# Kernel tuning notes

Hardware: AMD Instinct MI355X
Metric: run time of the kernel (lower is better)

## Reference

```python
import jax, jax.numpy as jnp
import numpy as np

NUM_REGIONS = 32  # region ids 1..32; id 0 is background, excluded like torch.unique()[ids>0]


def setup_inputs() -> dict:
    key = jax.random.key(0)
    k1, k2 = jax.random.split(key)
    B, T, C, D, H, W = 2, 8, 64, 48, 48, 48
    features = jax.random.normal(k1, (B, T, C, D, H, W), dtype=jnp.float32)
    segmentation = jax.random.randint(k2, (B, 1, D, H, W), 0, NUM_REGIONS + 1, dtype=jnp.int32)
    return {"features": features, "segmentation": segmentation}


def reference(features, segmentation):
    # features: [B, T, C, D, H, W], segmentation: [B, 1, D, H, W] (int region ids)
    B, T, C, D, H, W = features.shape
    N = D * H * W
    seg = segmentation.reshape(B, N)                 # [B, N]
    feats = features.reshape(B, T, C, N)             # [B, T, C, N]

    def per_batch(f, s):
        # f: [T, C, N], s: [N]
        fv = f.reshape(T * C, N).T                   # [N, T*C] voxel-major
        sums = jax.ops.segment_sum(fv, s, num_segments=NUM_REGIONS + 1)          # [R+1, T*C]
        counts = jax.ops.segment_sum(jnp.ones((N,), f.dtype), s,
                                     num_segments=NUM_REGIONS + 1)               # [R+1]
        # mean per region; empty regions stay zero (torch code `continue`s, leaving zeros)
        means = jnp.where(counts[:, None] > 0,
                          sums / jnp.maximum(counts, 1.0)[:, None],
                          0.0)
        return means[1:].reshape(NUM_REGIONS, T, C).transpose(1, 0, 2)           # [T, R, C]

    return jax.vmap(per_batch)(feats, seg)          # [B, T, num_regions, feature_dim]
```

## Files before the change

### kernel.cpp

```cpp
#include <hip/hip_runtime.h>


#define BB 2
#define TT 8
#define CC 64
#define NVOX 110592
#define NREG 32
#define RS 33
#define TS 67
#define WTILE (16*TS)
#define WACC (RS*CC)
#define WLDS (WTILE+WACC)
#define VPW 256
#define CHUNKV 1024

__global__ __launch_bounds__(256) void seg_hist(const int* __restrict__ seg,
                                                float* __restrict__ counts) {
    __shared__ float h[4 * RS];
    const int tid = threadIdx.x;
    const int w = tid >> 6;
    for (int i = tid; i < 4 * RS; i += 256) h[i] = 0.f;
    __syncthreads();

    const int base = blockIdx.x * 1024 + tid * 4;
    const int b = base / NVOX;
    const int4 s4 = *(const int4*)(seg + base);
    atomicAdd(&h[w * RS + s4.x], 1.f);
    atomicAdd(&h[w * RS + s4.y], 1.f);
    atomicAdd(&h[w * RS + s4.z], 1.f);
    atomicAdd(&h[w * RS + s4.w], 1.f);
    __syncthreads();

    if (tid < RS) {
        const float v = h[tid] + h[RS + tid] + h[2 * RS + tid] + h[3 * RS + tid];
        atomicAdd(&counts[b * RS + tid], v);
    }
}

__global__ __launch_bounds__(256) void seg_sum(const float* __restrict__ feat,
                                               const int* __restrict__ seg,
                                               float* __restrict__ out) {
    __shared__ float s[4 * WLDS];
    const int tid = threadIdx.x;
    const int w = tid >> 6;
    const int l = tid & 63;
    const int b = blockIdx.z;
    const int t = blockIdx.y;

    float* __restrict__ tile = s + w * WLDS;
    float* __restrict__ acc = tile + WTILE;
    #pragma unroll
    for (int i = l; i < WACC; i += 64) acc[i] = 0.f;

    const int v0 = blockIdx.x * CHUNKV + w * VPW;
    const int cq = l >> 2;
    const int iq = l & 3;
    const float* __restrict__ fbt = feat + (size_t)(b * TT + t) * CC * NVOX + v0;
    const float* __restrict__ fp0 = fbt + (size_t)(cq) * NVOX + iq * 4;
    const float* __restrict__ fp1 = fbt + (size_t)(cq + 16) * NVOX + iq * 4;
    const float* __restrict__ fp2 = fbt + (size_t)(cq + 32) * NVOX + iq * 4;
    const float* __restrict__ fp3 = fbt + (size_t)(cq + 48) * NVOX + iq * 4;
    const int* __restrict__ sb = seg + (size_t)b * NVOX + v0;

    const int wb = (iq * 4) * TS + cq;

    #pragma unroll 2
    for (int tj = 0; tj < 16; ++tj) {
        const int vo = tj * 16;
        const float4 f0 = *(const float4*)(fp0 + vo);
        const float4 f1 = *(const float4*)(fp1 + vo);
        const float4 f2 = *(const float4*)(fp2 + vo);
        const float4 f3 = *(const float4*)(fp3 + vo);
        const int4 s0 = *(const int4*)(sb + vo);
        const int4 s1 = *(const int4*)(sb + vo + 4);
        const int4 s2 = *(const int4*)(sb + vo + 8);
        const int4 s3 = *(const int4*)(sb + vo + 12);

        __builtin_amdgcn_wave_barrier();
        tile[wb] = f0.x;           tile[wb + TS] = f0.y;
        tile[wb + 2 * TS] = f0.z;  tile[wb + 3 * TS] = f0.w;
        tile[wb + 16] = f1.x;          tile[wb + 16 + TS] = f1.y;
        tile[wb + 16 + 2 * TS] = f1.z; tile[wb + 16 + 3 * TS] = f1.w;
        tile[wb + 32] = f2.x;          tile[wb + 32 + TS] = f2.y;
        tile[wb + 32 + 2 * TS] = f2.z; tile[wb + 32 + 3 * TS] = f2.w;
        tile[wb + 48] = f3.x;          tile[wb + 48 + TS] = f3.y;
        tile[wb + 48 + 2 * TS] = f3.z; tile[wb + 48 + 3 * TS] = f3.w;
        __builtin_amdgcn_wave_barrier();

        const int rv[16] = {s0.x, s0.y, s0.z, s0.w, s1.x, s1.y, s1.z, s1.w,
                            s2.x, s2.y, s2.z, s2.w, s3.x, s3.y, s3.z, s3.w};
        #pragma unroll
        for (int v = 0; v < 16; ++v) {
            const float val = tile[v * TS + l];
            acc[(rv[v] << 6) + l] += val;
        }
    }
    __syncthreads();

    float* __restrict__ outbt = out + (size_t)(b * TT + t) * NREG * CC;
    for (int i = tid; i < NREG * CC; i += 256) {
        const int off = WTILE + ((i >> 6) + 1) * CC + (i & 63);
        const float v = s[off] + s[WLDS + off] + s[2 * WLDS + off] + s[3 * WLDS + off];
        atomicAdd(&outbt[i], v);
    }
}

__global__ __launch_bounds__(256) void seg_div(float* __restrict__ out,
                                               const float* __restrict__ counts) {
    const int i = blockIdx.x * 256 + threadIdx.x;
    const int b = i >> 14;
    const int r = ((i >> 6) & 31) + 1;
    const float cnt = counts[b * RS + r];
    const float v = out[i];
    out[i] = cnt > 0.f ? v / cnt : 0.f;
}

extern "C" void kernel_launch(void* const* d_in, const int* in_sizes, int n_in,
                              void* d_out, int out_size, void* d_ws, size_t ws_size,
                              hipStream_t stream) {
    const float* feat = (const float*)d_in[0];
    const int* seg = (const int*)d_in[1];
    float* out = (float*)d_out;
    float* counts = (float*)d_ws;

    hipMemsetAsync(d_out, 0, (size_t)out_size * sizeof(float), stream);
    hipMemsetAsync(d_ws, 0, (size_t)(BB * RS) * sizeof(float), stream);

    seg_hist<<<dim3((BB * NVOX) / 1024), 256, 0, stream>>>(seg, counts);
    seg_sum<<<dim3(NVOX / CHUNKV, TT, BB), 256, 0, stream>>>(feat, seg, out);
    seg_div<<<dim3(out_size / 256), 256, 0, stream>>>(out, counts);
}
```

Baseline: 608.1 us.

## Replace per-wave LDS transpose with shared block accumulator using LDS atomics

Removes the per-wave LDS transpose tile and the four private per-wave accumulators. Each lane now atomically adds its feature values straight into one block-wide padded region×channel accumulator held in LDS. This cuts LDS footprint, which can raise occupancy, and drops the transpose stores, reads and the final four-way reduction. The cost is float LDS atomics with likely contention, since 33 regions are shared by all 256 threads.

Result: slower. 1.045 ms (+71.9%).

```diff
diff --git a/kernel.cpp b/kernel.cpp
--- a/kernel.cpp
+++ b/kernel.cpp
@@ -7,10 +7,8 @@
 #define NVOX 110592
 #define NREG 32
 #define RS 33
-#define TS 67
-#define WTILE (16*TS)
-#define WACC (RS*CC)
-#define WLDS (WTILE+WACC)
+#define PAD 65
+#define WACC (RS * PAD)
 #define VPW 256
 #define CHUNKV 1024
 
@@ -40,29 +38,24 @@
 __global__ __launch_bounds__(256) void seg_sum(const float* __restrict__ feat,
                                                const int* __restrict__ seg,
                                                float* __restrict__ out) {
-    __shared__ float s[4 * WLDS];
+    __shared__ float acc[WACC];
     const int tid = threadIdx.x;
-    const int w = tid >> 6;
     const int l = tid & 63;
     const int b = blockIdx.z;
     const int t = blockIdx.y;
 
-    float* __restrict__ tile = s + w * WLDS;
-    float* __restrict__ acc = tile + WTILE;
-    #pragma unroll
-    for (int i = l; i < WACC; i += 64) acc[i] = 0.f;
+    for (int i = tid; i < WACC; i += 256) acc[i] = 0.f;
+    __syncthreads();
 
-    const int v0 = blockIdx.x * CHUNKV + w * VPW;
+    const int v0 = blockIdx.x * CHUNKV + (tid >> 6) * VPW;
     const int cq = l >> 2;
     const int iq = l & 3;
-    const float* __restrict__ fbt = feat + (size_t)(b * TT + t) * CC * NVOX + v0;
-    const float* __restrict__ fp0 = fbt + (size_t)(cq) * NVOX + iq * 4;
-    const float* __restrict__ fp1 = fbt + (size_t)(cq + 16) * NVOX + iq * 4;
-    const float* __restrict__ fp2 = fbt + (size_t)(cq + 32) * NVOX + iq * 4;
-    const float* __restrict__ fp3 = fbt + (size_t)(cq + 48) * NVOX + iq * 4;
-    const int* __restrict__ sb = seg + (size_t)b * NVOX + v0;
-
-    const int wb = (iq * 4) * TS + cq;
+    const float* __restrict__ fp0 = feat + (size_t)(b * TT + t) * CC * NVOX
+                                    + (size_t)cq * NVOX + v0 + iq * 4;
+    const float* __restrict__ fp1 = fp0 + (size_t)16 * NVOX;
+    const float* __restrict__ fp2 = fp0 + (size_t)32 * NVOX;
+    const float* __restrict__ fp3 = fp0 + (size_t)48 * NVOX;
+    const int* __restrict__ sb = seg + (size_t)b * NVOX + v0 + iq * 4;
 
     #pragma unroll 2
     for (int tj = 0; tj < 16; ++tj) {
@@ -71,37 +64,26 @@
         const float4 f1 = *(const float4*)(fp1 + vo);
         const float4 f2 = *(const float4*)(fp2 + vo);
         const float4 f3 = *(const float4*)(fp3 + vo);
-        const int4 s0 = *(const int4*)(sb + vo);
-        const int4 s1 = *(const int4*)(sb + vo + 4);
-        const int4 s2 = *(const int4*)(sb + vo + 8);
-        const int4 s3 = *(const int4*)(sb + vo + 12);
+        const int4 s4 = *(const int4*)(sb + vo);
 
-        __builtin_amdgcn_wave_barrier();
-        tile[wb] = f0.x;           tile[wb + TS] = f0.y;
-        tile[wb + 2 * TS] = f0.z;  tile[wb + 3 * TS] = f0.w;
-        tile[wb + 16] = f1.x;          tile[wb + 16 + TS] = f1.y;
-        tile[wb + 16 + 2 * TS] = f1.z; tile[wb + 16 + 3 * TS] = f1.w;
-        tile[wb + 32] = f2.x;          tile[wb + 32 + TS] = f2.y;
-        tile[wb + 32 + 2 * TS] = f2.z; tile[wb + 32 + 3 * TS] = f2.w;
-        tile[wb + 48] = f3.x;          tile[wb + 48 + TS] = f3.y;
-        tile[wb + 48 + 2 * TS] = f3.z; tile[wb + 48 + 3 * TS] = f3.w;
-        __builtin_amdgcn_wave_barrier();
-
-        const int rv[16] = {s0.x, s0.y, s0.z, s0.w, s1.x, s1.y, s1.z, s1.w,
-                            s2.x, s2.y, s2.z, s2.w, s3.x, s3.y, s3.z, s3.w};
-        #pragma unroll
-        for (int v = 0; v < 16; ++v) {
-            const float val = tile[v * TS + l];
-            acc[(rv[v] << 6) + l] += val;
-        }
+        float* const a0 = acc + s4.x * PAD + cq;
+        float* const a1 = acc + s4.y * PAD + cq;
+        float* const a2 = acc + s4.z * PAD + cq;
+        float* const a3 = acc + s4.w * PAD + cq;
+        atomicAdd(a0,      f0.x); atomicAdd(a0 + 16, f1.x);
+        atomicAdd(a0 + 32, f2.x); atomicAdd(a0 + 48, f3.x);
+        atomicAdd(a1,      f0.y); atomicAdd(a1 + 16, f1.y);
+        atomicAdd(a1 + 32, f2.y); atomicAdd(a1 + 48, f3.y);
+        atomicAdd(a2,      f0.z); atomicAdd(a2 + 16, f1.z);
+        atomicAdd(a2 + 32, f2.z); atomicAdd(a2 + 48, f3.z);
+        atomicAdd(a3,      f0.w); atomicAdd(a3 + 16, f1.w);
+        atomicAdd(a3 + 32, f2.w); atomicAdd(a3 + 48, f3.w);
     }
     __syncthreads();
 
     float* __restrict__ outbt = out + (size_t)(b * TT + t) * NREG * CC;
     for (int i = tid; i < NREG * CC; i += 256) {
-        const int off = WTILE + ((i >> 6) + 1) * CC + (i & 63);
-        const float v = s[off] + s[WLDS + off] + s[2 * WLDS + off] + s[3 * WLDS + off];
-        atomicAdd(&outbt[i], v);
+        atomicAdd(&outbt[i], acc[((i >> 6) + 1) * PAD + (i & 63)]);
     }
 }
 
```
